# Kernel tuning notes

Hardware: AMD Instinct MI355X
Metric: run time of the kernel (lower is better)

Reference implementation:

```python
import jax, jax.numpy as jnp
import numpy as np

EPS = 1e-5

def ln(x, gamma, beta):
    m = jnp.mean(x, axis=-1, keepdims=True)
    std = jnp.sqrt(jnp.var(x, axis=-1, keepdims=True) + EPS)
    return gamma * ((x - m) / (std + EPS)) + beta

def hard_sigmoid(x):
    return jnp.clip(0.2 * x + 0.5, 0.0, 1.0)

def setup_inputs() -> dict:
    key = jax.random.key(0)
    B, T, D, U, UEP = 64, 2048, 256, 256, 64
    ks = jax.random.split(key, 16)
    def gn(k, shape, s=0.05):
        return (jax.random.normal(k, shape, dtype=jnp.float32) * s)
    inp = {}
    inp['x'] = jax.random.normal(ks[0], (B, T, D), dtype=jnp.float32)
    inp['mask'] = jax.random.randint(ks[1], (B, T), 0, 2, dtype=jnp.int32)
    inp['W'] = gn(ks[2], (D, 3 * U))
    inp['U'] = gn(ks[3], (U, 3 * U))
    inp['b'] = jnp.zeros((3 * U,), jnp.float32)
    inp['gammas'] = 1.0 + gn(ks[4], (2, 3 * U), 0.1)
    inp['betas'] = gn(ks[5], (2, 3 * U), 0.1)
    inp['W_EP'] = gn(ks[6], (D, 3 * UEP))
    inp['U_EP'] = gn(ks[7], (UEP, 3 * UEP))
    inp['b_EP'] = jnp.zeros((3 * UEP,), jnp.float32)
    inp['gammas_EP'] = 1.0 + gn(ks[8], (2, 3 * UEP), 0.1)
    inp['betas_EP'] = gn(ks[9], (2, 3 * UEP), 0.1)
    inp['W1_EP'] = gn(ks[10], (UEP, 1))
    inp['b1_EP'] = jnp.zeros((1,), jnp.float32)
    return inp

def _gru_step(s1, h_tm1, Umat, g1, bt1, dim):
    # s1: precomputed ln(x@W + b)  [B, 3*dim]
    s2 = ln(h_tm1 @ Umat[:, :2 * dim], g1[:2 * dim], bt1[:2 * dim])
    s = hard_sigmoid(s1[:, :2 * dim] + s2)
    z, r = s[:, :dim], s[:, dim:2 * dim]
    hh = ln((r * h_tm1) @ Umat[:, 2 * dim:], g1[2 * dim:], bt1[2 * dim:])
    return z * h_tm1 + (1.0 - z) * jnp.tanh(s1[:, 2 * dim:] + hh)

def _encoder(x, mask, W, U, b, gammas, betas, W_EP, U_EP, b_EP, gammas_EP, betas_EP, W1_EP, b1_EP):
    B, T, D = x.shape
    dim = U.shape[0]
    dim_ep = U_EP.shape[0]
    # input projections + their LayerNorms depend only on x -> precompute (same math)
    s1_all = ln(jnp.einsum('btd,dk->btk', x, W) + b, gammas[0], betas[0])          # [B,T,3U]
    s1_ep_all = ln(jnp.einsum('btd,dk->btk', x, W_EP) + b_EP, gammas_EP[0], betas_EP[0])  # [B,T,3Uep]
    s1_all = jnp.swapaxes(s1_all, 0, 1)        # [T,B,3U]
    s1_ep_all = jnp.swapaxes(s1_ep_all, 0, 1)  # [T,B,3Uep]
    xm_all = (mask > 0).T                      # [T,B] bool

    def step(carry, inp):
        h_tm1, hep_tm1, is_end_tm1 = carry
        s1, s1e, xm = inp
        h_tm1 = jnp.where(is_end_tm1[:, None] > 0.5, 0.0, h_tm1)
        h = _gru_step(s1, h_tm1, U, gammas[1], betas[1], dim)
        h = jnp.where(xm[:, None], h, h_tm1)
        hep = _gru_step(s1e, hep_tm1, U_EP, gammas_EP[1], betas_EP[1], dim_ep)
        hep = jnp.where(xm[:, None], hep, hep_tm1)
        is_end = jnp.round(jax.nn.sigmoid(hep_tm1 @ W1_EP + b1_EP))[:, 0]
        return (h, hep, is_end), (h, is_end)

    init = (jnp.zeros((B, dim), x.dtype), jnp.zeros((B, dim_ep), x.dtype), jnp.zeros((B,), x.dtype))
    _, (h_seq, end_seq) = jax.lax.scan(step, init, (s1_all, s1_ep_all, xm_all))
    return jnp.swapaxes(h_seq, 0, 1), jnp.swapaxes(end_seq, 0, 1)  # [B,T,U], [B,T]

def reference(x, mask, W, U, b, gammas, betas, W_EP, U_EP, b_EP, gammas_EP, betas_EP, W1_EP, b1_EP):
    return _encoder(x, mask, W, U, b, gammas, betas, W_EP, U_EP, b_EP, gammas_EP, betas_EP, W1_EP, b1_EP)
```

## Files before the change

### kernel.cpp

```cpp
#include <hip/hip_runtime.h>


typedef _Float16 h2  __attribute__((ext_vector_type(2)));
typedef _Float16 v8h __attribute__((ext_vector_type(8)));

__device__ __forceinline__ float fdot2_(h2 a, h2 b, float c) {
#if __has_builtin(__builtin_amdgcn_fdot2)
  return __builtin_amdgcn_fdot2(a, b, c, false);
#else
  return c + (float)a[0] * (float)b[0] + (float)a[1] * (float)b[1];
#endif
}

template <int I>
__device__ __forceinline__ h2 pr(v8h v) {
  h2 r; r[0] = v[2 * I]; r[1] = v[2 * I + 1]; return r;
}

__device__ __forceinline__ void wg_barrier() {
  __builtin_amdgcn_sched_barrier(0);
  asm volatile("s_waitcnt lgkmcnt(0)" ::: "memory");
  __builtin_amdgcn_sched_barrier(0);
  __builtin_amdgcn_s_barrier();
  __builtin_amdgcn_sched_barrier(0);
}

__global__ __launch_bounds__(256) void prep_kernel(
    const float* __restrict__ W, const float* __restrict__ U,
    const float* __restrict__ W_EP,
    _Float16* __restrict__ wt, _Float16* __restrict__ uzr,
    _Float16* __restrict__ uh, float* __restrict__ wept)
{
  const int blk = blockIdx.x;
  const int k = threadIdx.x;
  if (blk < 768) {
    const int j = blk;
    wt[(size_t)j * 256 + k] = (_Float16)W[(size_t)k * 768 + j];
  } else if (blk < 1280) {
    const int j = blk - 768;
    uzr[(size_t)j * 256 + k] = (_Float16)U[(size_t)k * 768 + j];
  } else if (blk < 1536) {
    const int j = blk - 1280;
    const int p = k >> 3, e = k & 7;
    uh[((size_t)p * 256 + j) * 8 + e] = (_Float16)U[(size_t)k * 768 + 512 + j];
  } else {
    const int j = blk - 1536;
    wept[(size_t)j * 256 + k] = W_EP[(size_t)k * 192 + j];
  }
}

__global__ __launch_bounds__(256) void ph1_main_kernel(
    const float* __restrict__ x, const _Float16* __restrict__ wt,
    const float* __restrict__ bvec, const float* __restrict__ gam,
    const float* __restrict__ bet, _Float16* __restrict__ s1out)
{
  __shared__ __align__(16) _Float16 xs[16][256];
  __shared__ float sp[16][768];
  const int tid = threadIdx.x;
  const size_t row0 = (size_t)blockIdx.x * 16;

  #pragma unroll
  for (int i = 0; i < 16; ++i)
    xs[i][tid] = (_Float16)x[(row0 + i) * 256 + tid];
  __syncthreads();

  #pragma unroll 1
  for (int cc = 0; cc < 3; ++cc) {
    const int col = cc * 256 + tid;
    const v8h* wp = (const v8h*)(wt + (size_t)col * 256);
    float acc[16];
    #pragma unroll
    for (int r = 0; r < 16; ++r) acc[r] = 0.f;
    #pragma unroll 4
    for (int c = 0; c < 32; ++c) {
      const v8h w8 = wp[c];
      #pragma unroll
      for (int r = 0; r < 16; ++r) {
        const v8h x8 = *(const v8h*)(&xs[r][c * 8]);
        acc[r] = fdot2_(pr<0>(x8), pr<0>(w8), acc[r]);
        acc[r] = fdot2_(pr<1>(x8), pr<1>(w8), acc[r]);
        acc[r] = fdot2_(pr<2>(x8), pr<2>(w8), acc[r]);
        acc[r] = fdot2_(pr<3>(x8), pr<3>(w8), acc[r]);
      }
    }
    const float bb = bvec[col];
    #pragma unroll
    for (int r = 0; r < 16; ++r) sp[r][col] = acc[r] + bb;
  }
  __syncthreads();

  const int w = tid >> 6, lane = tid & 63;
  for (int rr = 0; rr < 4; ++rr) {
    const int r = (w << 2) | rr;
    float vals[12], sum = 0.f, sq = 0.f;
    #pragma unroll
    for (int j = 0; j < 12; ++j) {
      const float v = sp[r][lane + (j << 6)];
      vals[j] = v; sum += v; sq += v * v;
    }
    #pragma unroll
    for (int m = 32; m >= 1; m >>= 1) {
      sum += __shfl_xor(sum, m); sq += __shfl_xor(sq, m);
    }
    const float mean = sum * (1.f / 768.f);
    const float var = sq * (1.f / 768.f) - mean * mean;
    const float inv = 1.f / (sqrtf(var + 1e-5f) + 1e-5f);
    #pragma unroll
    for (int j = 0; j < 12; ++j) {
      const int c = lane + (j << 6);
      s1out[(row0 + r) * 768 + c] =
          (_Float16)(gam[c] * ((vals[j] - mean) * inv) + bet[c]);
    }
  }
}

__global__ __launch_bounds__(192) void ph1_ep_kernel(
    const float* __restrict__ x, const float* __restrict__ wept,
    const float* __restrict__ bvec, const float* __restrict__ gam,
    const float* __restrict__ bet, void* __restrict__ s1e, const int store64)
{
  __shared__ __align__(16) float xs[16][256];
  __shared__ double sp[16][192];
  const int tid = threadIdx.x;
  const size_t row0 = (size_t)blockIdx.x * 16;

  for (int idx = tid; idx < 4096; idx += 192)
    xs[idx >> 8][idx & 255] = x[row0 * 256 + idx];
  __syncthreads();

  {
    const float4* wp = (const float4*)(wept + (size_t)tid * 256);
    double acc[16];
    #pragma unroll
    for (int r = 0; r < 16; ++r) acc[r] = 0.0;
    #pragma unroll 2
    for (int c = 0; c < 64; ++c) {
      const float4 w4 = wp[c];
      #pragma unroll
      for (int r = 0; r < 16; ++r) {
        const float4 x4 = *(const float4*)(&xs[r][c * 4]);
        acc[r] += (double)x4.x * (double)w4.x;
        acc[r] += (double)x4.y * (double)w4.y;
        acc[r] += (double)x4.z * (double)w4.z;
        acc[r] += (double)x4.w * (double)w4.w;
      }
    }
    const double bb = (double)bvec[tid];
    #pragma unroll
    for (int r = 0; r < 16; ++r) sp[r][tid] = acc[r] + bb;
  }
  __syncthreads();

  const int w = tid >> 6, lane = tid & 63;
  for (int r = w; r < 16; r += 3) {
    double vals[3], sum = 0.0, sq = 0.0;
    #pragma unroll
    for (int j = 0; j < 3; ++j) {
      const double v = sp[r][lane + (j << 6)];
      vals[j] = v; sum += v; sq += v * v;
    }
    #pragma unroll
    for (int m = 32; m >= 1; m >>= 1) {
      sum += __shfl_xor(sum, m); sq += __shfl_xor(sq, m);
    }
    const double mean = sum * (1.0 / 192.0);
    const double var = sq * (1.0 / 192.0) - mean * mean;
    const double den = sqrt(var + 1e-5) + 1e-5;
    #pragma unroll
    for (int j = 0; j < 3; ++j) {
      const int c = lane + (j << 6);
      const double vv = (double)gam[c] * ((vals[j] - mean) / den) + (double)bet[c];
      if (store64) ((double*)s1e)[(row0 + r) * 192 + c] = vv;
      else         ((float*)s1e)[(row0 + r) * 192 + c] = (float)vv;
    }
  }
}

#define OFF_UH     0
#define OFF_MASK   131072
#define OFF_HEP    139264
#define OFF_ZEE    139776
#define OFF_RHEP   140288
#define OFF_EPZRP  140800
#define OFF_EPHHP  140928
#define OFF_H2     140992
#define OFF_RH     141504
#define OFF_HF     142016
#define OFF_Z      143040
#define OFF_ZRP    144064
#define OFF_HHP    144128
#define OFF_FLAG   144160
#define SCAN_LDS_BYTES 144192

__global__ __launch_bounds__(512, 2) void scan_kernel(
    const _Float16* __restrict__ uzr_g, const _Float16* __restrict__ uh_g,
    const float* __restrict__ U_EP, const _Float16* __restrict__ s1,
    const void* __restrict__ s1e_v, const int s1e64,
    const int* __restrict__ mask,
    const float* __restrict__ gam1, const float* __restrict__ bet1,
    const float* __restrict__ gamep1, const float* __restrict__ betep1,
    const float* __restrict__ W1, const float* __restrict__ b1,
    float* __restrict__ out)
{
  extern __shared__ char sm[];
  const int t = threadIdx.x;
  const int b = blockIdx.x;
  const int w = t >> 6;
  const int je  = t >> 2;
  const int qe  = t & 3;
  const int jeh = (t & 255) >> 2;

  float*  hf    = (float*)(sm + OFF_HF);
  float*  flagp = (float*)(sm + OFF_FLAG);
  double* hepd  = (double*)(sm + OFF_HEP);
  int*    maskl = (int*)(sm + OFF_MASK);

  {
    const v8h* src = (const v8h*)uh_g;
    v8h* dst = (v8h*)(sm + OFF_UH);
    #pragma unroll
    for (int i = 0; i < 16; ++i) dst[i * 512 + t] = src[i * 512 + t];
  }
  #pragma unroll
  for (int i = 0; i < 4; ++i) maskl[i * 512 + t] = mask[((size_t)b << 11) + i * 512 + t];

  v8h uzrv[32];
  {
    const v8h* up = (const v8h*)uzr_g + (size_t)t * 32;
    #pragma unroll
    for (int c = 0; c < 32; ++c) uzrv[c] = up[c];
  }
  float uez[16], ueh[16];
  #pragma unroll
  for (int i = 0; i < 16; ++i) uez[i] = U_EP[(size_t)(16 * qe + i) * 192 + je];
  #pragma unroll
  for (int i = 0; i < 16; ++i) ueh[i] = U_EP[(size_t)(16 * qe + i) * 192 + 128 + jeh];

  const float gz = gam1[t],                bz = bet1[t];
  const float gh = gam1[512 + (t & 255)],  bh = bet1[512 + (t & 255)];
  const float gse = gamep1[je],            bse = betep1[je];
  const float ghe = gamep1[128 + jeh],     bhe = betep1[128 + jeh];
  const double w1d = (double)W1[t & 63];
  const double b1d = (double)b1[0];
  const double* dptr = (const double*)s1e_v;
  const float*  fptr = (const float*)s1e_v;

  if (t < 128) { h2 z2; z2[0] = (_Float16)0.f; z2[1] = (_Float16)0.f;
                 ((h2*)(sm + OFF_H2))[t] = z2; }
  if (t < 256) hf[t] = 0.f;
  if (t < 64)  hepd[t] = 0.0;
  if (t < 2)   flagp[t] = 0.f;

  const size_t n0 = (size_t)b << 11;
  float  s1zr_c = (float)s1[n0 * 768 + t];
  float  s1h_c  = (float)s1[n0 * 768 + 512 + (t & 255)];
  double s1ezr_c = s1e64 ? dptr[n0 * 192 + je]
                         : (double)fptr[n0 * 192 + je];
  double s1ehh_c = s1e64 ? dptr[n0 * 192 + 128 + jeh]
                         : (double)fptr[n0 * 192 + 128 + jeh];
  __syncthreads();

  for (int tt = 0; tt < 2048; ++tt) {
    const size_t n = ((size_t)b << 11) | (size_t)tt;
    const float fz = (flagp[tt & 1] > 0.5f) ? 0.f : 1.f;

    if (tt > 0 && t < 256) out[(n - 1) * 256 + t] = hf[t];

    const int ttn = (tt < 2047) ? tt + 1 : 2047;
    const size_t np1 = ((size_t)b << 11) | (size_t)ttn;
    const float  s1zr_n = (float)s1[np1 * 768 + t];
    const float  s1h_n  = (float)s1[np1 * 768 + 512 + (t & 255)];
    const double s1ezr_n = s1e64 ? dptr[np1 * 192 + je]
                                 : (double)fptr[np1 * 192 + je];
    const double s1ehh_n = s1e64 ? dptr[np1 * 192 + 128 + jeh]
                                 : (double)fptr[np1 * 192 + 128 + jeh];

    if (w == 7) {
      double p = hepd[t & 63] * w1d;
      #pragma unroll
      for (int m = 1; m <= 32; m <<= 1) p += __shfl_xor(p, m);
      if (t == 448) {
        const float e = ((p + b1d) > 0.0) ? 1.f : 0.f;
        flagp[(tt + 1) & 1] = e;
        out[(size_t)33554432 + n] = e;
      }
    }

    float d;
    {
      const v8h* hv = (const v8h*)(sm + OFF_H2);
      float a0 = 0.f, a1 = 0.f, a2 = 0.f, a3 = 0.f;
      #pragma unroll
      for (int c = 0; c < 32; ++c) {
        const v8h hc = hv[c];
        a0 = fdot2_(pr<0>(hc), pr<0>(uzrv[c]), a0);
        a1 = fdot2_(pr<1>(hc), pr<1>(uzrv[c]), a1);
        a2 = fdot2_(pr<2>(hc), pr<2>(uzrv[c]), a2);
        a3 = fdot2_(pr<3>(hc), pr<3>(uzrv[c]), a3);
      }
      d = ((a0 + a1) + (a2 + a3)) * fz;
      float s_ = d, q_ = d * d;
      #pragma unroll
      for (int m = 1; m <= 32; m <<= 1) { s_ += __shfl_xor(s_, m); q_ += __shfl_xor(q_, m); }
      if ((t & 63) == 0) ((float2*)(sm + OFF_ZRP))[w] = make_float2(s_, q_);
    }
    double de;
    {
      const double2* hp = (const double2*)(hepd + 16 * qe);
      double acc = 0.0;
      #pragma unroll
      for (int i = 0; i < 8; ++i) {
        const double2 hv2 = hp[i];
        acc += hv2.x * (double)uez[2 * i] + hv2.y * (double)uez[2 * i + 1];
      }
      acc += __shfl_xor(acc, 1); acc += __shfl_xor(acc, 2);
      de = acc;
      double es = de, eq = de * de;
      #pragma unroll
      for (int m = 4; m <= 32; m <<= 1) { es += __shfl_xor(es, m); eq += __shfl_xor(eq, m); }
      if ((t & 63) == 0) ((double2*)(sm + OFF_EPZRP))[w] = make_double2(es, eq);
    }
    wg_barrier();

    {
      float S = 0.f, Q = 0.f;
      const float4* zp = (const float4*)(sm + OFF_ZRP);
      #pragma unroll
      for (int i = 0; i < 4; ++i) { const float4 v = zp[i]; S += v.x + v.z; Q += v.y + v.w; }
      const float mean = S * (1.f / 512.f);
      const float var = Q * (1.f / 512.f) - mean * mean;
      const float inv = 1.f / (sqrtf(var + 1e-5f) + 1e-5f);
      const float s2v = gz * ((d - mean) * inv) + bz;
      float sv = 0.2f * (s1zr_c + s2v) + 0.5f;
      sv = fminf(fmaxf(sv, 0.f), 1.f);
      if (t < 256) ((float*)(sm + OFF_Z))[t] = sv;
      else {
        const float rhv = sv * (fz * hf[t - 256]);
        ((_Float16*)(sm + OFF_RH))[t - 256] = (_Float16)rhv;
      }
    }
    if ((t & 3) == 0) {
      double S = 0.0, Q = 0.0;
      const double2* ep = (const double2*)(sm + OFF_EPZRP);
      #pragma unroll
      for (int i = 0; i < 8; ++i) { S += ep[i].x; Q += ep[i].y; }
      const double mean = S * (1.0 / 128.0);
      const double var = Q * (1.0 / 128.0) - mean * mean;
      const double den = sqrt(var + 1e-5) + 1e-5;
      const double s2e = (double)gse * ((de - mean) / den) + (double)bse;
      double se = 0.2 * (s1ezr_c + s2e) + 0.5;
      se = fmin(fmax(se, 0.0), 1.0);
      if (je < 64) ((double*)(sm + OFF_ZEE))[je] = se;
      else         ((double*)(sm + OFF_RHEP))[je - 64] = se * hepd[je - 64];
    }
    wg_barrier();

    float dh = 0.f;
    double deh = 0.0;
    if (t < 256) {
      const v8h* rhv8 = (const v8h*)(sm + OFF_RH);
      const v8h* uhv  = (const v8h*)(sm + OFF_UH);
      float c0 = 0.f, c1 = 0.f, c2 = 0.f, c3 = 0.f;
      #pragma unroll
      for (int p = 0; p < 32; ++p) {
        const v8h rc = rhv8[p];
        const v8h uc = uhv[p * 256 + t];
        c0 = fdot2_(pr<0>(rc), pr<0>(uc), c0);
        c1 = fdot2_(pr<1>(rc), pr<1>(uc), c1);
        c2 = fdot2_(pr<2>(rc), pr<2>(uc), c2);
        c3 = fdot2_(pr<3>(rc), pr<3>(uc), c3);
      }
      dh = (c0 + c1) + (c2 + c3);
      float s_ = dh, q_ = dh * dh;
      #pragma unroll
      for (int m = 1; m <= 32; m <<= 1) { s_ += __shfl_xor(s_, m); q_ += __shfl_xor(q_, m); }
      if ((t & 63) == 0) ((float2*)(sm + OFF_HHP))[w] = make_float2(s_, q_);
    } else {
      const double2* rp = (const double2*)((double*)(sm + OFF_RHEP) + 16 * qe);
      double acc = 0.0;
      #pragma unroll
      for (int i = 0; i < 8; ++i) {
        const double2 rv = rp[i];
        acc += rv.x * (double)ueh[2 * i] + rv.y * (double)ueh[2 * i + 1];
      }
      acc += __shfl_xor(acc, 1); acc += __shfl_xor(acc, 2);
      deh = acc;
      double es = deh, eq = deh * deh;
      #pragma unroll
      for (int m = 4; m <= 32; m <<= 1) { es += __shfl_xor(es, m); eq += __shfl_xor(eq, m); }
      if ((t & 63) == 0) ((double2*)(sm + OFF_EPHHP))[w - 4] = make_double2(es, eq);
    }
    wg_barrier();

    const int xm = maskl[tt];
    if (t < 256) {
      float S = 0.f, Q = 0.f;
      const float4* hp4 = (const float4*)(sm + OFF_HHP);
      #pragma unroll
      for (int i = 0; i < 2; ++i) { const float4 v = hp4[i]; S += v.x + v.z; Q += v.y + v.w; }
      const float mean = S * (1.f / 256.f);
      const float var = Q * (1.f / 256.f) - mean * mean;
      const float inv = 1.f / (sqrtf(var + 1e-5f) + 1e-5f);
      const float hhv = gh * ((dh - mean) * inv) + bh;
      const float z = ((float*)(sm + OFF_Z))[t];
      const float hzf = fz * hf[t];
      const float hn = z * hzf + (1.f - z) * tanhf(s1h_c + hhv);
      const float hc_ = (xm > 0) ? hn : hzf;
      hf[t] = hc_;
      const float ho = __shfl_xor(hc_, 1);
      if (!(t & 1)) {
        h2 p2; p2[0] = (_Float16)hc_; p2[1] = (_Float16)ho;
        ((h2*)(sm + OFF_H2))[t >> 1] = p2;
      }
    } else if ((t & 3) == 0) {
      double S = 0.0, Q = 0.0;
      const double2* ep = (const double2*)(sm + OFF_EPHHP);
      #pragma unroll
      for (int i = 0; i < 4; ++i) { S += ep[i].x; Q += ep[i].y; }
      const double mean = S * (1.0 / 64.0);
      const double var = Q * (1.0 / 64.0) - mean * mean;
      const double den = sqrt(var + 1e-5) + 1e-5;
      const double hhe = (double)ghe * ((deh - mean) / den) + (double)bhe;
      const double ze = ((double*)(sm + OFF_ZEE))[jeh];
      const double hold = hepd[jeh];
      const double hepn = ze * hold + (1.0 - ze) * tanh(s1ehh_c + hhe);
      hepd[jeh] = (xm > 0) ? hepn : hold;
    }
    wg_barrier();

    s1zr_c = s1zr_n; s1h_c = s1h_n; s1ezr_c = s1ezr_n; s1ehh_c = s1ehh_n;
  }
  if (t < 256) out[((((size_t)b << 11) | 2047)) * 256 + t] = hf[t];
}

extern "C" void kernel_launch(void* const* d_in, const int* in_sizes, int n_in,
                              void* d_out, int out_size, void* d_ws, size_t ws_size,
                              hipStream_t stream)
{
  (void)in_sizes; (void)n_in; (void)out_size;
  const float* x       = (const float*)d_in[0];
  const int*   mask    = (const int*)d_in[1];
  const float* W       = (const float*)d_in[2];
  const float* U       = (const float*)d_in[3];
  const float* bvec    = (const float*)d_in[4];
  const float* gammas  = (const float*)d_in[5];
  const float* betas   = (const float*)d_in[6];
  const float* W_EP    = (const float*)d_in[7];
  const float* U_EP    = (const float*)d_in[8];
  const float* b_EP    = (const float*)d_in[9];
  const float* gammasE = (const float*)d_in[10];
  const float* betasE  = (const float*)d_in[11];
  const float* W1_EP   = (const float*)d_in[12];
  const float* b1_EP   = (const float*)d_in[13];
  float* out = (float*)d_out;

  const size_t NR = 131072;
  const size_t S1_SZ    = NR * 768 * 2;
  const size_t S1E64_SZ = NR * 192 * 8;
  const size_t S1E32_SZ = NR * 192 * 4;
  const size_t WSMALL = 262144 + 131072 + 393216 + 196608;
  const int s1e64 = (ws_size >= S1_SZ + S1E64_SZ + WSMALL) ? 1 : 0;
  const size_t S1E_SZ = s1e64 ? S1E64_SZ : S1E32_SZ;
  if (ws_size < S1_SZ + S1E32_SZ + WSMALL) return;

  char* ws = (char*)d_ws;
  size_t off = 0;
  void* s1e      = (void*)(ws + off);      off += S1E_SZ;
  _Float16* s1   = (_Float16*)(ws + off);  off += S1_SZ;
  _Float16* uzr  = (_Float16*)(ws + off);  off += 262144;
  _Float16* uh   = (_Float16*)(ws + off);  off += 131072;
  _Float16* wt   = (_Float16*)(ws + off);  off += 393216;
  float* wept    = (float*)(ws + off);     off += 196608;

  prep_kernel<<<dim3(1728), dim3(256), 0, stream>>>(
      W, U, W_EP, wt, uzr, uh, wept);
  ph1_main_kernel<<<dim3(8192), dim3(256), 0, stream>>>(
      x, wt, bvec, gammas, betas, s1);
  ph1_ep_kernel<<<dim3(8192), dim3(192), 0, stream>>>(
      x, wept, b_EP, gammasE, betasE, s1e, s1e64);

  hipFuncSetAttribute(reinterpret_cast<const void*>(scan_kernel),
                      hipFuncAttributeMaxDynamicSharedMemorySize, SCAN_LDS_BYTES);
  scan_kernel<<<dim3(64), dim3(512), SCAN_LDS_BYTES, stream>>>(
      uzr, uh, U_EP, s1, (const void*)s1e, s1e64, mask,
      gammas + 768, betas + 768, gammasE + 192, betasE + 192,
      W1_EP, b1_EP, out);
}
```

Before: 20.75 ms.

## Stream recurrent weights from global each step and broadcast hidden state via readlane

The 512-lane register cache of the z/r recurrent weights (32 v8h per thread) is dropped. Each step now reloads those weights from global/L2 in two halves of 16 vectors, interleaved with the EP dot product and the end-flag computation. The hidden state and r*h vectors are read once per lane from LDS and broadcast with readlane, replacing repeated LDS vector loads. This frees a large block of VGPRs, but it adds per-step global traffic on the serial critical path and many scalar readlane operations.

```diff
diff --git a/kernel.cpp b/kernel.cpp
--- a/kernel.cpp
+++ b/kernel.cpp
@@ -15,6 +15,10 @@
 template <int I>
 __device__ __forceinline__ h2 pr(v8h v) {
   h2 r; r[0] = v[2 * I]; r[1] = v[2 * I + 1]; return r;
+}
+
+__device__ __forceinline__ h2 rl2(int wreg, int k) {
+  return __builtin_bit_cast(h2, __builtin_amdgcn_readlane(wreg, k));
 }
 
 __device__ __forceinline__ void wg_barrier() {
@@ -206,6 +210,7 @@
   const int t = threadIdx.x;
   const int b = blockIdx.x;
   const int w = t >> 6;
+  const int lane = t & 63;
   const int je  = t >> 2;
   const int qe  = t & 3;
   const int jeh = (t & 255) >> 2;
@@ -224,12 +229,6 @@
   #pragma unroll
   for (int i = 0; i < 4; ++i) maskl[i * 512 + t] = mask[((size_t)b << 11) + i * 512 + t];
 
-  v8h uzrv[32];
-  {
-    const v8h* up = (const v8h*)uzr_g + (size_t)t * 32;
-    #pragma unroll
-    for (int c = 0; c < 32; ++c) uzrv[c] = up[c];
-  }
   float uez[16], ueh[16];
   #pragma unroll
   for (int i = 0; i < 16; ++i) uez[i] = U_EP[(size_t)(16 * qe + i) * 192 + je];
@@ -240,10 +239,11 @@
   const float gh = gam1[512 + (t & 255)],  bh = bet1[512 + (t & 255)];
   const float gse = gamep1[je],            bse = betep1[je];
   const float ghe = gamep1[128 + jeh],     bhe = betep1[128 + jeh];
-  const double w1d = (double)W1[t & 63];
+  const double w1d = (double)W1[lane];
   const double b1d = (double)b1[0];
   const double* dptr = (const double*)s1e_v;
   const float*  fptr = (const float*)s1e_v;
+  const v8h* up = (const v8h*)uzr_g + (size_t)t * 32;
 
   if (t < 128) { h2 z2; z2[0] = (_Float16)0.f; z2[1] = (_Float16)0.f;
                  ((h2*)(sm + OFF_H2))[t] = z2; }
@@ -266,6 +266,10 @@
 
     if (tt > 0 && t < 256) out[(n - 1) * 256 + t] = hf[t];
 
+    v8h wz[16];
+    #pragma unroll
+    for (int c = 0; c < 16; ++c) wz[c] = up[c];
+
     const int ttn = (tt < 2047) ? tt + 1 : 2047;
     const size_t np1 = ((size_t)b << 11) | (size_t)ttn;
     const float  s1zr_n = (float)s1[np1 * 768 + t];
@@ -275,41 +279,35 @@
     const double s1ehh_n = s1e64 ? dptr[np1 * 192 + 128 + jeh]
                                  : (double)fptr[np1 * 192 + 128 + jeh];
 
-    if (w == 7) {
-      double p = hepd[t & 63] * w1d;
-      #pragma unroll
-      for (int m = 1; m <= 32; m <<= 1) p += __shfl_xor(p, m);
-      if (t == 448) {
-        const float e = ((p + b1d) > 0.0) ? 1.f : 0.f;
-        flagp[(tt + 1) & 1] = e;
-        out[(size_t)33554432 + n] = e;
-      }
-    }
-
-    float d;
-    {
-      const v8h* hv = (const v8h*)(sm + OFF_H2);
-      float a0 = 0.f, a1 = 0.f, a2 = 0.f, a3 = 0.f;
-      #pragma unroll
-      for (int c = 0; c < 32; ++c) {
-        const v8h hc = hv[c];
-        a0 = fdot2_(pr<0>(hc), pr<0>(uzrv[c]), a0);
-        a1 = fdot2_(pr<1>(hc), pr<1>(uzrv[c]), a1);
-        a2 = fdot2_(pr<2>(hc), pr<2>(uzrv[c]), a2);
-        a3 = fdot2_(pr<3>(hc), pr<3>(uzrv[c]), a3);
-      }
-      d = ((a0 + a1) + (a2 + a3)) * fz;
-      float s_ = d, q_ = d * d;
-      #pragma unroll
-      for (int m = 1; m <= 32; m <<= 1) { s_ += __shfl_xor(s_, m); q_ += __shfl_xor(q_, m); }
-      if ((t & 63) == 0) ((float2*)(sm + OFF_ZRP))[w] = make_float2(s_, q_);
-    }
+    const int* h2i = (const int*)(sm + OFF_H2);
+    const int hw0 = h2i[lane];
+    const int hw1 = h2i[64 + lane];
+
     double de;
     {
       const double2* hp = (const double2*)(hepd + 16 * qe);
       double acc = 0.0;
       #pragma unroll
-      for (int i = 0; i < 8; ++i) {
+      for (int i = 0; i < 4; ++i) {
+        const double2 hv2 = hp[i];
+        acc += hv2.x * (double)uez[2 * i] + hv2.y * (double)uez[2 * i + 1];
+      }
+
+      float a0 = 0.f, a1 = 0.f, a2 = 0.f, a3 = 0.f;
+      #pragma unroll
+      for (int c = 0; c < 16; ++c) {
+        const v8h wv = wz[c];
+        a0 = fdot2_(rl2(hw0, 4 * c + 0), pr<0>(wv), a0);
+        a1 = fdot2_(rl2(hw0, 4 * c + 1), pr<1>(wv), a1);
+        a2 = fdot2_(rl2(hw0, 4 * c + 2), pr<2>(wv), a2);
+        a3 = fdot2_(rl2(hw0, 4 * c + 3), pr<3>(wv), a3);
+      }
+
+      #pragma unroll
+      for (int c = 0; c < 16; ++c) wz[c] = up[16 + c];
+
+      #pragma unroll
+      for (int i = 4; i < 8; ++i) {
         const double2 hv2 = hp[i];
         acc += hv2.x * (double)uez[2 * i] + hv2.y * (double)uez[2 * i + 1];
       }
@@ -318,63 +316,99 @@
       double es = de, eq = de * de;
       #pragma unroll
       for (int m = 4; m <= 32; m <<= 1) { es += __shfl_xor(es, m); eq += __shfl_xor(eq, m); }
-      if ((t & 63) == 0) ((double2*)(sm + OFF_EPZRP))[w] = make_double2(es, eq);
-    }
-    wg_barrier();
-
-    {
-      float S = 0.f, Q = 0.f;
-      const float4* zp = (const float4*)(sm + OFF_ZRP);
-      #pragma unroll
-      for (int i = 0; i < 4; ++i) { const float4 v = zp[i]; S += v.x + v.z; Q += v.y + v.w; }
-      const float mean = S * (1.f / 512.f);
-      const float var = Q * (1.f / 512.f) - mean * mean;
-      const float inv = 1.f / (sqrtf(var + 1e-5f) + 1e-5f);
-      const float s2v = gz * ((d - mean) * inv) + bz;
-      float sv = 0.2f * (s1zr_c + s2v) + 0.5f;
-      sv = fminf(fmaxf(sv, 0.f), 1.f);
-      if (t < 256) ((float*)(sm + OFF_Z))[t] = sv;
-      else {
-        const float rhv = sv * (fz * hf[t - 256]);
-        ((_Float16*)(sm + OFF_RH))[t - 256] = (_Float16)rhv;
-      }
-    }
-    if ((t & 3) == 0) {
-      double S = 0.0, Q = 0.0;
-      const double2* ep = (const double2*)(sm + OFF_EPZRP);
-      #pragma unroll
-      for (int i = 0; i < 8; ++i) { S += ep[i].x; Q += ep[i].y; }
-      const double mean = S * (1.0 / 128.0);
-      const double var = Q * (1.0 / 128.0) - mean * mean;
-      const double den = sqrt(var + 1e-5) + 1e-5;
-      const double s2e = (double)gse * ((de - mean) / den) + (double)bse;
-      double se = 0.2 * (s1ezr_c + s2e) + 0.5;
-      se = fmin(fmax(se, 0.0), 1.0);
-      if (je < 64) ((double*)(sm + OFF_ZEE))[je] = se;
-      else         ((double*)(sm + OFF_RHEP))[je - 64] = se * hepd[je - 64];
+      if (lane == 0) ((double2*)(sm + OFF_EPZRP))[w] = make_double2(es, eq);
+
+      if (w == 7) {
+        double p = hepd[lane] * w1d;
+        #pragma unroll
+        for (int m = 1; m <= 32; m <<= 1) p += __shfl_xor(p, m);
+        if (t == 448) {
+          const float e = ((p + b1d) > 0.0) ? 1.f : 0.f;
+          flagp[(tt + 1) & 1] = e;
+          out[(size_t)33554432 + n] = e;
+        }
+      }
+
+      #pragma unroll
+      for (int c = 0; c < 16; ++c) {
+        const v8h wv = wz[c];
+        a0 = fdot2_(rl2(hw1, 4 * c + 0), pr<0>(wv), a0);
+        a1 = fdot2_(rl2(hw1, 4 * c + 1), pr<1>(wv), a1);
+        a2 = fdot2_(rl2(hw1, 4 * c + 2), pr<2>(wv), a2);
+        a3 = fdot2_(rl2(hw1, 4 * c + 3), pr<3>(wv), a3);
+      }
+      const float d_ = ((a0 + a1) + (a2 + a3)) * fz;
+      float s_ = d_, q_ = d_ * d_;
+      #pragma unroll
+      for (int m = 1; m <= 32; m <<= 1) { s_ += __shfl_xor(s_, m); q_ += __shfl_xor(q_, m); }
+      if (lane == 0) ((float2*)(sm + OFF_ZRP))[w] = make_float2(s_, q_);
+
+      s_ = d_;
+      wg_barrier();
+
+      {
+        float S = 0.f, Q = 0.f;
+        const float4* zp = (const float4*)(sm + OFF_ZRP);
+        #pragma unroll
+        for (int i = 0; i < 4; ++i) { const float4 v = zp[i]; S += v.x + v.z; Q += v.y + v.w; }
+        const float mean = S * (1.f / 512.f);
+        const float var = Q * (1.f / 512.f) - mean * mean;
+        const float inv = 1.f / (sqrtf(var + 1e-5f) + 1e-5f);
+        const float s2v = gz * ((d_ - mean) * inv) + bz;
+        float sv = 0.2f * (s1zr_c + s2v) + 0.5f;
+        sv = fminf(fmaxf(sv, 0.f), 1.f);
+        if (t < 256) ((float*)(sm + OFF_Z))[t] = sv;
+        else {
+          const float rhv = sv * (fz * hf[t - 256]);
+          ((_Float16*)(sm + OFF_RH))[t - 256] = (_Float16)rhv;
+        }
+      }
+      if ((t & 3) == 0) {
+        double S = 0.0, Q = 0.0;
+        const double2* ep = (const double2*)(sm + OFF_EPZRP);
+        #pragma unroll
+        for (int i = 0; i < 8; ++i) { S += ep[i].x; Q += ep[i].y; }
+        const double mean = S * (1.0 / 128.0);
+        const double var = Q * (1.0 / 128.0) - mean * mean;
+        const double den = sqrt(var + 1e-5) + 1e-5;
+        const double s2e = (double)gse * ((de - mean) / den) + (double)bse;
+        double se = 0.2 * (s1ezr_c + s2e) + 0.5;
+        se = fmin(fmax(se, 0.0), 1.0);
+        if (je < 64) ((double*)(sm + OFF_ZEE))[je] = se;
+        else         ((double*)(sm + OFF_RHEP))[je - 64] = se * hepd[je - 64];
+      }
     }
     wg_barrier();
 
     float dh = 0.f;
     double deh = 0.0;
     if (t < 256) {
-      const v8h* rhv8 = (const v8h*)(sm + OFF_RH);
-      const v8h* uhv  = (const v8h*)(sm + OFF_UH);
+      const int* rhi = (const int*)(sm + OFF_RH);
+      const int rr0 = rhi[lane];
+      const int rr1 = rhi[64 + lane];
+      const v8h* uhv = (const v8h*)(sm + OFF_UH);
       float c0 = 0.f, c1 = 0.f, c2 = 0.f, c3 = 0.f;
       #pragma unroll
-      for (int p = 0; p < 32; ++p) {
-        const v8h rc = rhv8[p];
+      for (int p = 0; p < 16; ++p) {
         const v8h uc = uhv[p * 256 + t];
-        c0 = fdot2_(pr<0>(rc), pr<0>(uc), c0);
-        c1 = fdot2_(pr<1>(rc), pr<1>(uc), c1);
-        c2 = fdot2_(pr<2>(rc), pr<2>(uc), c2);
-        c3 = fdot2_(pr<3>(rc), pr<3>(uc), c3);
+        c0 = fdot2_(rl2(rr0, 4 * p + 0), pr<0>(uc), c0);
+        c1 = fdot2_(rl2(rr0, 4 * p + 1), pr<1>(uc), c1);
+        c2 = fdot2_(rl2(rr0, 4 * p + 2), pr<2>(uc), c2);
+        c3 = fdot2_(rl2(rr0, 4 * p + 3), pr<3>(uc), c3);
+      }
+      #pragma unroll
+      for (int p = 16; p < 32; ++p) {
+        const v8h uc = uhv[p * 256 + t];
+        c0 = fdot2_(rl2(rr1, 4 * (p - 16) + 0), pr<0>(uc), c0);
+        c1 = fdot2_(rl2(rr1, 4 * (p - 16) + 1), pr<1>(uc), c1);
+        c2 = fdot2_(rl2(rr1, 4 * (p - 16) + 2), pr<2>(uc), c2);
+        c3 = fdot2_(rl2(rr1, 4 * (p - 16) + 3), pr<3>(uc), c3);
       }
       dh = (c0 + c1) + (c2 + c3);
       float s_ = dh, q_ = dh * dh;
       #pragma unroll
       for (int m = 1; m <= 32; m <<= 1) { s_ += __shfl_xor(s_, m); q_ += __shfl_xor(q_, m); }
-      if ((t & 63) == 0) ((float2*)(sm + OFF_HHP))[w] = make_float2(s_, q_);
+      if (lane == 0) ((float2*)(sm + OFF_HHP))[w] = make_float2(s_, q_);
     } else {
       const double2* rp = (const double2*)((double*)(sm + OFF_RHEP) + 16 * qe);
       double acc = 0.0;
@@ -388,7 +422,7 @@
       double es = deh, eq = deh * deh;
       #pragma unroll
       for (int m = 4; m <= 32; m <<= 1) { es += __shfl_xor(es, m); eq += __shfl_xor(eq, m); }
-      if ((t & 63) == 0) ((double2*)(sm + OFF_EPHHP))[w - 4] = make_double2(es, eq);
+      if (lane == 0) ((double2*)(sm + OFF_EPHHP))[w - 4] = make_double2(es, eq);
     }
     wg_barrier();
 
```

New measurement: 16.76 ms. 19.2% less time.

## Halve scan workgroup to 256 threads, stream U_zr weights from global each step

Applied to the files above, without the earlier changes.

The recurrent scan kernel now runs with 256 threads instead of 512. Each thread computes both the z and r gate columns, and the EP path handles two gate columns per thread. The U_zr weights are no longer held in registers. They are re-read from global memory (L2) every timestep through a software-pipelined triple-buffered load/dot sequence, using a new interleaved layout. The aim is to cut barrier and cross-wave reduction cost per step with fewer waves. The tradeoff is double the per-thread dot-product work and weight bandwidth on the serial critical path.

```diff
diff --git a/kernel.cpp b/kernel.cpp
--- a/kernel.cpp
+++ b/kernel.cpp
@@ -23,6 +23,32 @@
   __builtin_amdgcn_sched_barrier(0);
   __builtin_amdgcn_s_barrier();
   __builtin_amdgcn_sched_barrier(0);
+}
+
+template <int K>
+__device__ __forceinline__ void ldblk(v8h* d, const v8h* base, int tz, int tr) {
+  #pragma unroll
+  for (int i = 0; i < 4; ++i) {
+    d[i]     = base[(size_t)(4 * K + i) * 512 + tz];
+    d[4 + i] = base[(size_t)(4 * K + i) * 512 + tr];
+  }
+}
+template <int K>
+__device__ __forceinline__ void dotblk(const v8h* hv, const v8h* d,
+    float& za0, float& za1, float& za2, float& za3,
+    float& ra0, float& ra1, float& ra2, float& ra3) {
+  #pragma unroll
+  for (int i = 0; i < 4; ++i) {
+    const v8h hc = hv[4 * K + i];
+    za0 = fdot2_(pr<0>(hc), pr<0>(d[i]), za0);
+    za1 = fdot2_(pr<1>(hc), pr<1>(d[i]), za1);
+    za2 = fdot2_(pr<2>(hc), pr<2>(d[i]), za2);
+    za3 = fdot2_(pr<3>(hc), pr<3>(d[i]), za3);
+    ra0 = fdot2_(pr<0>(hc), pr<0>(d[4 + i]), ra0);
+    ra1 = fdot2_(pr<1>(hc), pr<1>(d[4 + i]), ra1);
+    ra2 = fdot2_(pr<2>(hc), pr<2>(d[4 + i]), ra2);
+    ra3 = fdot2_(pr<3>(hc), pr<3>(d[4 + i]), ra3);
+  }
 }
 
 __global__ __launch_bounds__(256) void prep_kernel(
@@ -38,7 +64,8 @@
     wt[(size_t)j * 256 + k] = (_Float16)W[(size_t)k * 768 + j];
   } else if (blk < 1280) {
     const int j = blk - 768;
-    uzr[(size_t)j * 256 + k] = (_Float16)U[(size_t)k * 768 + j];
+    const int c = k >> 3, e = k & 7;
+    uzr[((size_t)c * 512 + j) * 8 + e] = (_Float16)U[(size_t)k * 768 + j];
   } else if (blk < 1536) {
     const int j = blk - 1280;
     const int p = k >> 3, e = k & 7;
@@ -186,13 +213,12 @@
 #define OFF_H2     140992
 #define OFF_RH     141504
 #define OFF_HF     142016
-#define OFF_Z      143040
 #define OFF_ZRP    144064
 #define OFF_HHP    144128
 #define OFF_FLAG   144160
 #define SCAN_LDS_BYTES 144192
 
-__global__ __launch_bounds__(512, 2) void scan_kernel(
+__global__ __launch_bounds__(256, 1) void scan_kernel(
     const _Float16* __restrict__ uzr_g, const _Float16* __restrict__ uh_g,
     const float* __restrict__ U_EP, const _Float16* __restrict__ s1,
     const void* __restrict__ s1e_v, const int s1e64,
@@ -206,9 +232,9 @@
   const int t = threadIdx.x;
   const int b = blockIdx.x;
   const int w = t >> 6;
+  const int lane = t & 63;
+  const int qe  = t & 3;
   const int je  = t >> 2;
-  const int qe  = t & 3;
-  const int jeh = (t & 255) >> 2;
 
   float*  hf    = (float*)(sm + OFF_HF);
   float*  flagp = (float*)(sm + OFF_FLAG);
@@ -219,145 +245,157 @@
     const v8h* src = (const v8h*)uh_g;
     v8h* dst = (v8h*)(sm + OFF_UH);
     #pragma unroll
-    for (int i = 0; i < 16; ++i) dst[i * 512 + t] = src[i * 512 + t];
-  }
-  #pragma unroll
-  for (int i = 0; i < 4; ++i) maskl[i * 512 + t] = mask[((size_t)b << 11) + i * 512 + t];
-
-  v8h uzrv[32];
-  {
-    const v8h* up = (const v8h*)uzr_g + (size_t)t * 32;
-    #pragma unroll
-    for (int c = 0; c < 32; ++c) uzrv[c] = up[c];
-  }
-  float uez[16], ueh[16];
-  #pragma unroll
-  for (int i = 0; i < 16; ++i) uez[i] = U_EP[(size_t)(16 * qe + i) * 192 + je];
-  #pragma unroll
-  for (int i = 0; i < 16; ++i) ueh[i] = U_EP[(size_t)(16 * qe + i) * 192 + 128 + jeh];
-
-  const float gz = gam1[t],                bz = bet1[t];
-  const float gh = gam1[512 + (t & 255)],  bh = bet1[512 + (t & 255)];
-  const float gse = gamep1[je],            bse = betep1[je];
-  const float ghe = gamep1[128 + jeh],     bhe = betep1[128 + jeh];
-  const double w1d = (double)W1[t & 63];
+    for (int i = 0; i < 32; ++i) dst[i * 256 + t] = src[i * 256 + t];
+  }
+  #pragma unroll
+  for (int i = 0; i < 8; ++i) maskl[i * 256 + t] = mask[((size_t)b << 11) + i * 256 + t];
+
+  float uezA[16], uezB[16], ueh[16];
+  #pragma unroll
+  for (int i = 0; i < 16; ++i) uezA[i] = U_EP[(size_t)(16 * qe + i) * 192 + je];
+  #pragma unroll
+  for (int i = 0; i < 16; ++i) uezB[i] = U_EP[(size_t)(16 * qe + i) * 192 + 64 + je];
+  #pragma unroll
+  for (int i = 0; i < 16; ++i) ueh[i] = U_EP[(size_t)(16 * qe + i) * 192 + 128 + je];
+
+  const float gz  = gam1[t],        bz  = bet1[t];
+  const float gzr = gam1[256 + t],  bzr = bet1[256 + t];
+  const float gh  = gam1[512 + t],  bh  = bet1[512 + t];
+  const float gseA = gamep1[je],       bseA = betep1[je];
+  const float gseB = gamep1[64 + je],  bseB = betep1[64 + je];
+  const float ghe  = gamep1[128 + je], bhe  = betep1[128 + je];
+  const double w1d = (double)W1[lane];
   const double b1d = (double)b1[0];
   const double* dptr = (const double*)s1e_v;
   const float*  fptr = (const float*)s1e_v;
 
   if (t < 128) { h2 z2; z2[0] = (_Float16)0.f; z2[1] = (_Float16)0.f;
                  ((h2*)(sm + OFF_H2))[t] = z2; }
-  if (t < 256) hf[t] = 0.f;
+  hf[t] = 0.f;
   if (t < 64)  hepd[t] = 0.0;
   if (t < 2)   flagp[t] = 0.f;
 
   const size_t n0 = (size_t)b << 11;
-  float  s1zr_c = (float)s1[n0 * 768 + t];
-  float  s1h_c  = (float)s1[n0 * 768 + 512 + (t & 255)];
-  double s1ezr_c = s1e64 ? dptr[n0 * 192 + je]
-                         : (double)fptr[n0 * 192 + je];
-  double s1ehh_c = s1e64 ? dptr[n0 * 192 + 128 + jeh]
-                         : (double)fptr[n0 * 192 + 128 + jeh];
+  float  s1zA_c = (float)s1[n0 * 768 + t];
+  float  s1zB_c = (float)s1[n0 * 768 + 256 + t];
+  float  s1h_c  = (float)s1[n0 * 768 + 512 + t];
+  double s1eA_c = s1e64 ? dptr[n0 * 192 + je]      : (double)fptr[n0 * 192 + je];
+  double s1eB_c = s1e64 ? dptr[n0 * 192 + 64 + je] : (double)fptr[n0 * 192 + 64 + je];
+  double s1eh_c = s1e64 ? dptr[n0 * 192 + 128 + je]: (double)fptr[n0 * 192 + 128 + je];
   __syncthreads();
 
   for (int tt = 0; tt < 2048; ++tt) {
     const size_t n = ((size_t)b << 11) | (size_t)tt;
     const float fz = (flagp[tt & 1] > 0.5f) ? 0.f : 1.f;
 
-    if (tt > 0 && t < 256) out[(n - 1) * 256 + t] = hf[t];
+    if (tt > 0) out[(n - 1) * 256 + t] = hf[t];
 
     const int ttn = (tt < 2047) ? tt + 1 : 2047;
     const size_t np1 = ((size_t)b << 11) | (size_t)ttn;
-    const float  s1zr_n = (float)s1[np1 * 768 + t];
-    const float  s1h_n  = (float)s1[np1 * 768 + 512 + (t & 255)];
-    const double s1ezr_n = s1e64 ? dptr[np1 * 192 + je]
-                                 : (double)fptr[np1 * 192 + je];
-    const double s1ehh_n = s1e64 ? dptr[np1 * 192 + 128 + jeh]
-                                 : (double)fptr[np1 * 192 + 128 + jeh];
-
-    if (w == 7) {
-      double p = hepd[t & 63] * w1d;
+    const float  s1zA_n = (float)s1[np1 * 768 + t];
+    const float  s1zB_n = (float)s1[np1 * 768 + 256 + t];
+    const float  s1h_n  = (float)s1[np1 * 768 + 512 + t];
+    const double s1eA_n = s1e64 ? dptr[np1 * 192 + je]       : (double)fptr[np1 * 192 + je];
+    const double s1eB_n = s1e64 ? dptr[np1 * 192 + 64 + je]  : (double)fptr[np1 * 192 + 64 + je];
+    const double s1eh_n = s1e64 ? dptr[np1 * 192 + 128 + je] : (double)fptr[np1 * 192 + 128 + je];
+
+    const v8h* uzb = (const v8h*)uzr_g;
+    asm volatile("" : "+v"(uzb));
+    v8h A[8], Bv[8], Cv[8];
+    ldblk<0>(A, uzb, t, 256 + t);
+    ldblk<1>(Bv, uzb, t, 256 + t);
+    ldblk<2>(Cv, uzb, t, 256 + t);
+
+    const v8h* hv = (const v8h*)(sm + OFF_H2);
+    float za0 = 0.f, za1 = 0.f, za2 = 0.f, za3 = 0.f;
+    float ra0 = 0.f, ra1 = 0.f, ra2 = 0.f, ra3 = 0.f;
+    dotblk<0>(hv, A,  za0, za1, za2, za3, ra0, ra1, ra2, ra3);
+    ldblk<3>(A, uzb, t, 256 + t);
+    dotblk<1>(hv, Bv, za0, za1, za2, za3, ra0, ra1, ra2, ra3);
+    ldblk<4>(Bv, uzb, t, 256 + t);
+    dotblk<2>(hv, Cv, za0, za1, za2, za3, ra0, ra1, ra2, ra3);
+    ldblk<5>(Cv, uzb, t, 256 + t);
+    dotblk<3>(hv, A,  za0, za1, za2, za3, ra0, ra1, ra2, ra3);
+    ldblk<6>(A, uzb, t, 256 + t);
+    dotblk<4>(hv, Bv, za0, za1, za2, za3, ra0, ra1, ra2, ra3);
+    ldblk<7>(Bv, uzb, t, 256 + t);
+
+    double deA, deB;
+    {
+      const double2* hp = (const double2*)(hepd + 16 * qe);
+      double accA = 0.0, accB = 0.0;
+      #pragma unroll
+      for (int i = 0; i < 8; ++i) {
+        const double2 hv2 = hp[i];
+        accA += hv2.x * (double)uezA[2 * i] + hv2.y * (double)uezA[2 * i + 1];
+        accB += hv2.x * (double)uezB[2 * i] + hv2.y * (double)uezB[2 * i + 1];
+      }
+      accA += __shfl_xor(accA, 1); accA += __shfl_xor(accA, 2);
+      accB += __shfl_xor(accB, 1); accB += __shfl_xor(accB, 2);
+      deA = accA; deB = accB;
+      double es = deA + deB, eq = deA * deA + deB * deB;
+      #pragma unroll
+      for (int m = 4; m <= 32; m <<= 1) { es += __shfl_xor(es, m); eq += __shfl_xor(eq, m); }
+      if (lane == 0) ((double2*)(sm + OFF_EPZRP))[w] = make_double2(es, eq);
+    }
+    if (w == 3) {
+      double p = hepd[lane] * w1d;
       #pragma unroll
       for (int m = 1; m <= 32; m <<= 1) p += __shfl_xor(p, m);
-      if (t == 448) {
+      if (t == 192) {
         const float e = ((p + b1d) > 0.0) ? 1.f : 0.f;
         flagp[(tt + 1) & 1] = e;
         out[(size_t)33554432 + n] = e;
       }
     }
 
-    float d;
+    dotblk<5>(hv, Cv, za0, za1, za2, za3, ra0, ra1, ra2, ra3);
+    dotblk<6>(hv, A,  za0, za1, za2, za3, ra0, ra1, ra2, ra3);
+    dotblk<7>(hv, Bv, za0, za1, za2, za3, ra0, ra1, ra2, ra3);
+    const float dz = ((za0 + za1) + (za2 + za3)) * fz;
+    const float dr = ((ra0 + ra1) + (ra2 + ra3)) * fz;
     {
-      const v8h* hv = (const v8h*)(sm + OFF_H2);
-      float a0 = 0.f, a1 = 0.f, a2 = 0.f, a3 = 0.f;
-      #pragma unroll
-      for (int c = 0; c < 32; ++c) {
-        const v8h hc = hv[c];
-        a0 = fdot2_(pr<0>(hc), pr<0>(uzrv[c]), a0);
-        a1 = fdot2_(pr<1>(hc), pr<1>(uzrv[c]), a1);
-        a2 = fdot2_(pr<2>(hc), pr<2>(uzrv[c]), a2);
-        a3 = fdot2_(pr<3>(hc), pr<3>(uzrv[c]), a3);
-      }
-      d = ((a0 + a1) + (a2 + a3)) * fz;
-      float s_ = d, q_ = d * d;
+      float s_ = dz + dr, q_ = dz * dz + dr * dr;
       #pragma unroll
       for (int m = 1; m <= 32; m <<= 1) { s_ += __shfl_xor(s_, m); q_ += __shfl_xor(q_, m); }
-      if ((t & 63) == 0) ((float2*)(sm + OFF_ZRP))[w] = make_float2(s_, q_);
-    }
-    double de;
-    {
-      const double2* hp = (const double2*)(hepd + 16 * qe);
-      double acc = 0.0;
-      #pragma unroll
-      for (int i = 0; i < 8; ++i) {
-        const double2 hv2 = hp[i];
-        acc += hv2.x * (double)uez[2 * i] + hv2.y * (double)uez[2 * i + 1];
-      }
-      acc += __shfl_xor(acc, 1); acc += __shfl_xor(acc, 2);
-      de = acc;
-      double es = de, eq = de * de;
-      #pragma unroll
-      for (int m = 4; m <= 32; m <<= 1) { es += __shfl_xor(es, m); eq += __shfl_xor(eq, m); }
-      if ((t & 63) == 0) ((double2*)(sm + OFF_EPZRP))[w] = make_double2(es, eq);
+      if (lane == 0) ((float2*)(sm + OFF_ZRP))[w] = make_float2(s_, q_);
     }
     wg_barrier();
 
+    float zreg;
     {
       float S = 0.f, Q = 0.f;
       const float4* zp = (const float4*)(sm + OFF_ZRP);
       #pragma unroll
-      for (int i = 0; i < 4; ++i) { const float4 v = zp[i]; S += v.x + v.z; Q += v.y + v.w; }
+      for (int i = 0; i < 2; ++i) { const float4 v = zp[i]; S += v.x + v.z; Q += v.y + v.w; }
       const float mean = S * (1.f / 512.f);
       const float var = Q * (1.f / 512.f) - mean * mean;
       const float inv = 1.f / (sqrtf(var + 1e-5f) + 1e-5f);
-      const float s2v = gz * ((d - mean) * inv) + bz;
-      float sv = 0.2f * (s1zr_c + s2v) + 0.5f;
-      sv = fminf(fmaxf(sv, 0.f), 1.f);
-      if (t < 256) ((float*)(sm + OFF_Z))[t] = sv;
-      else {
-        const float rhv = sv * (fz * hf[t - 256]);
-        ((_Float16*)(sm + OFF_RH))[t - 256] = (_Float16)rhv;
-      }
-    }
-    if ((t & 3) == 0) {
+      float sz = 0.2f * (s1zA_c + (gz * ((dz - mean) * inv) + bz)) + 0.5f;
+      zreg = fminf(fmaxf(sz, 0.f), 1.f);
+      float sr = 0.2f * (s1zB_c + (gzr * ((dr - mean) * inv) + bzr)) + 0.5f;
+      sr = fminf(fmaxf(sr, 0.f), 1.f);
+      ((_Float16*)(sm + OFF_RH))[t] = (_Float16)(sr * (fz * hf[t]));
+    }
+    if (qe == 0) {
       double S = 0.0, Q = 0.0;
       const double2* ep = (const double2*)(sm + OFF_EPZRP);
       #pragma unroll
-      for (int i = 0; i < 8; ++i) { S += ep[i].x; Q += ep[i].y; }
+      for (int i = 0; i < 4; ++i) { S += ep[i].x; Q += ep[i].y; }
       const double mean = S * (1.0 / 128.0);
       const double var = Q * (1.0 / 128.0) - mean * mean;
       const double den = sqrt(var + 1e-5) + 1e-5;
-      const double s2e = (double)gse * ((de - mean) / den) + (double)bse;
-      double se = 0.2 * (s1ezr_c + s2e) + 0.5;
-      se = fmin(fmax(se, 0.0), 1.0);
-      if (je < 64) ((double*)(sm + OFF_ZEE))[je] = se;
-      else         ((double*)(sm + OFF_RHEP))[je - 64] = se * hepd[je - 64];
+      double seA = 0.2 * (s1eA_c + ((double)gseA * ((deA - mean) / den) + (double)bseA)) + 0.5;
+      seA = fmin(fmax(seA, 0.0), 1.0);
+      ((double*)(sm + OFF_ZEE))[je] = seA;
+      double seB = 0.2 * (s1eB_c + ((double)gseB * ((deB - mean) / den) + (double)bseB)) + 0.5;
+      seB = fmin(fmax(seB, 0.0), 1.0);
+      ((double*)(sm + OFF_RHEP))[je] = seB * hepd[je];
     }
     wg_barrier();
 
-    float dh = 0.f;
-    double deh = 0.0;
-    if (t < 256) {
+    float dh;
+    {
       const v8h* rhv8 = (const v8h*)(sm + OFF_RH);
       const v8h* uhv  = (const v8h*)(sm + OFF_UH);
       float c0 = 0.f, c1 = 0.f, c2 = 0.f, c3 = 0.f;
@@ -374,8 +412,10 @@
       float s_ = dh, q_ = dh * dh;
       #pragma unroll
       for (int m = 1; m <= 32; m <<= 1) { s_ += __shfl_xor(s_, m); q_ += __shfl_xor(q_, m); }
-      if ((t & 63) == 0) ((float2*)(sm + OFF_HHP))[w] = make_float2(s_, q_);
-    } else {
+      if (lane == 0) ((float2*)(sm + OFF_HHP))[w] = make_float2(s_, q_);
+    }
+    double deh;
+    {
       const double2* rp = (const double2*)((double*)(sm + OFF_RHEP) + 16 * qe);
       double acc = 0.0;
       #pragma unroll
@@ -388,12 +428,12 @@
       double es = deh, eq = deh * deh;
       #pragma unroll
       for (int m = 4; m <= 32; m <<= 1) { es += __shfl_xor(es, m); eq += __shfl_xor(eq, m); }
-      if ((t & 63) == 0) ((double2*)(sm + OFF_EPHHP))[w - 4] = make_double2(es, eq);
+      if (lane == 0) ((double2*)(sm + OFF_EPHHP))[w] = make_double2(es, eq);
     }
     wg_barrier();
 
     const int xm = maskl[tt];
-    if (t < 256) {
+    {
       float S = 0.f, Q = 0.f;
       const float4* hp4 = (const float4*)(sm + OFF_HHP);
       #pragma unroll
@@ -402,9 +442,8 @@
       const float var = Q * (1.f / 256.f) - mean * mean;
       const float inv = 1.f / (sqrtf(var + 1e-5f) + 1e-5f);
       const float hhv = gh * ((dh - mean) * inv) + bh;
-      const float z = ((float*)(sm + OFF_Z))[t];
       const float hzf = fz * hf[t];
-      const float hn = z * hzf + (1.f - z) * tanhf(s1h_c + hhv);
+      const float hn = zreg * hzf + (1.f - zreg) * tanhf(s1h_c + hhv);
       const float hc_ = (xm > 0) ? hn : hzf;
       hf[t] = hc_;
       const float ho = __shfl_xor(hc_, 1);
@@ -412,7 +451,8 @@
         h2 p2; p2[0] = (_Float16)hc_; p2[1] = (_Float16)ho;
         ((h2*)(sm + OFF_H2))[t >> 1] = p2;
       }
-    } else if ((t & 3) == 0) {
+    }
+    if (qe == 0) {
       double S = 0.0, Q = 0.0;
       const double2* ep = (const double2*)(sm + OFF_EPHHP);
       #pragma unroll
@@ -421,16 +461,17 @@
       const double var = Q * (1.0 / 64.0) - mean * mean;
       const double den = sqrt(var + 1e-5) + 1e-5;
       const double hhe = (double)ghe * ((deh - mean) / den) + (double)bhe;
-      const double ze = ((double*)(sm + OFF_ZEE))[jeh];
-      const double hold = hepd[jeh];
-      const double hepn = ze * hold + (1.0 - ze) * tanh(s1ehh_c + hhe);
-      hepd[jeh] = (xm > 0) ? hepn : hold;
+      const double ze = ((double*)(sm + OFF_ZEE))[je];
+      const double hold = hepd[je];
+      const double hepn = ze * hold + (1.0 - ze) * tanh(s1eh_c + hhe);
+      hepd[je] = (xm > 0) ? hepn : hold;
     }
     wg_barrier();
 
-    s1zr_c = s1zr_n; s1h_c = s1h_n; s1ezr_c = s1ezr_n; s1ehh_c = s1ehh_n;
-  }
-  if (t < 256) out[((((size_t)b << 11) | 2047)) * 256 + t] = hf[t];
+    s1zA_c = s1zA_n; s1zB_c = s1zB_n; s1h_c = s1h_n;
+    s1eA_c = s1eA_n; s1eB_c = s1eB_n; s1eh_c = s1eh_n;
+  }
+  out[((((size_t)b << 11) | 2047)) * 256 + t] = hf[t];
 }
 
 extern "C" void kernel_launch(void* const* d_in, const int* in_sizes, int n_in,
@@ -481,7 +522,7 @@
 
   hipFuncSetAttribute(reinterpret_cast<const void*>(scan_kernel),
                       hipFuncAttributeMaxDynamicSharedMemorySize, SCAN_LDS_BYTES);
-  scan_kernel<<<dim3(64), dim3(512), SCAN_LDS_BYTES, stream>>>(
+  scan_kernel<<<dim3(64), dim3(256), SCAN_LDS_BYTES, stream>>>(
       uzr, uh, U_EP, s1, (const void*)s1e, s1e64, mask,
       gammas + 768, betas + 768, gammasE + 192, betasE + 192,
       W1_EP, b1_EP, out);
```

Result: slower. 23.48 ms (+13.2%).

## Stream recurrent U_zr weights from global each step instead of holding in registers

Applied to the files above, without the earlier changes.

The 32 v8h recurrent z/r weight registers per thread are no longer kept resident. Each timestep instead streams them from global/L2 memory through an 8-entry double buffer, and the prep kernel reorders uzr into a coalesced chunk-major layout to suit this. The EP dot product is split and interleaved with the streamed loads to hide their latency. The aim is to cut register pressure, which may raise occupancy or avoid spills. The cost is reading about 256KB of weights per step per block, which adds L2 bandwidth demand and latency on the serial recurrence.

```diff
diff --git a/kernel.cpp b/kernel.cpp
--- a/kernel.cpp
+++ b/kernel.cpp
@@ -38,7 +38,8 @@
     wt[(size_t)j * 256 + k] = (_Float16)W[(size_t)k * 768 + j];
   } else if (blk < 1280) {
     const int j = blk - 768;
-    uzr[(size_t)j * 256 + k] = (_Float16)U[(size_t)k * 768 + j];
+    const int c = k >> 3, e = k & 7;
+    uzr[((size_t)c * 512 + j) * 8 + e] = (_Float16)U[(size_t)k * 768 + j];
   } else if (blk < 1536) {
     const int j = blk - 1280;
     const int p = k >> 3, e = k & 7;
@@ -224,12 +225,6 @@
   #pragma unroll
   for (int i = 0; i < 4; ++i) maskl[i * 512 + t] = mask[((size_t)b << 11) + i * 512 + t];
 
-  v8h uzrv[32];
-  {
-    const v8h* up = (const v8h*)uzr_g + (size_t)t * 32;
-    #pragma unroll
-    for (int c = 0; c < 32; ++c) uzrv[c] = up[c];
-  }
   float uez[16], ueh[16];
   #pragma unroll
   for (int i = 0; i < 16; ++i) uez[i] = U_EP[(size_t)(16 * qe + i) * 192 + je];
@@ -266,6 +261,15 @@
 
     if (tt > 0 && t < 256) out[(n - 1) * 256 + t] = hf[t];
 
+    const v8h* uzb = (const v8h*)uzr_g;
+    asm volatile("" : "+v"(uzb));
+
+    v8h wbuf[8];
+    #pragma unroll
+    for (int q = 0; q < 4; ++q) wbuf[q]     = uzb[(size_t)q * 512 + t];
+    #pragma unroll
+    for (int q = 0; q < 4; ++q) wbuf[4 + q] = uzb[(size_t)(4 + q) * 512 + t];
+
     const int ttn = (tt < 2047) ? tt + 1 : 2047;
     const size_t np1 = ((size_t)b << 11) | (size_t)ttn;
     const float  s1zr_n = (float)s1[np1 * 768 + t];
@@ -286,39 +290,57 @@
       }
     }
 
-    float d;
+    double de;
+    const double2* hp = (const double2*)(hepd + 16 * qe);
     {
-      const v8h* hv = (const v8h*)(sm + OFF_H2);
-      float a0 = 0.f, a1 = 0.f, a2 = 0.f, a3 = 0.f;
-      #pragma unroll
-      for (int c = 0; c < 32; ++c) {
-        const v8h hc = hv[c];
-        a0 = fdot2_(pr<0>(hc), pr<0>(uzrv[c]), a0);
-        a1 = fdot2_(pr<1>(hc), pr<1>(uzrv[c]), a1);
-        a2 = fdot2_(pr<2>(hc), pr<2>(uzrv[c]), a2);
-        a3 = fdot2_(pr<3>(hc), pr<3>(uzrv[c]), a3);
-      }
-      d = ((a0 + a1) + (a2 + a3)) * fz;
+      double acc = 0.0;
+      #pragma unroll
+      for (int i = 0; i < 4; ++i) {
+        const double2 hv2 = hp[i];
+        acc += hv2.x * (double)uez[2 * i] + hv2.y * (double)uez[2 * i + 1];
+      }
+      de = acc;
+    }
+
+    const v8h* hv = (const v8h*)(sm + OFF_H2);
+    float a0 = 0.f, a1 = 0.f, a2 = 0.f, a3 = 0.f;
+    #pragma unroll
+    for (int k = 0; k < 8; ++k) {
+      #pragma unroll
+      for (int i = 0; i < 4; ++i) {
+        const v8h hc = hv[4 * k + i];
+        const v8h wz = wbuf[(k & 1) * 4 + i];
+        a0 = fdot2_(pr<0>(hc), pr<0>(wz), a0);
+        a1 = fdot2_(pr<1>(hc), pr<1>(wz), a1);
+        a2 = fdot2_(pr<2>(hc), pr<2>(wz), a2);
+        a3 = fdot2_(pr<3>(hc), pr<3>(wz), a3);
+      }
+      if (k < 6) {
+        #pragma unroll
+        for (int q = 0; q < 4; ++q)
+          wbuf[(k & 1) * 4 + q] = uzb[(size_t)(4 * (k + 2) + q) * 512 + t];
+      }
+      if (k == 3) {
+        double acc = de;
+        #pragma unroll
+        for (int i = 4; i < 8; ++i) {
+          const double2 hv2 = hp[i];
+          acc += hv2.x * (double)uez[2 * i] + hv2.y * (double)uez[2 * i + 1];
+        }
+        acc += __shfl_xor(acc, 1); acc += __shfl_xor(acc, 2);
+        de = acc;
+        double es = de, eq = de * de;
+        #pragma unroll
+        for (int m = 4; m <= 32; m <<= 1) { es += __shfl_xor(es, m); eq += __shfl_xor(eq, m); }
+        if ((t & 63) == 0) ((double2*)(sm + OFF_EPZRP))[w] = make_double2(es, eq);
+      }
+    }
+    const float d = ((a0 + a1) + (a2 + a3)) * fz;
+    {
       float s_ = d, q_ = d * d;
       #pragma unroll
       for (int m = 1; m <= 32; m <<= 1) { s_ += __shfl_xor(s_, m); q_ += __shfl_xor(q_, m); }
       if ((t & 63) == 0) ((float2*)(sm + OFF_ZRP))[w] = make_float2(s_, q_);
-    }
-    double de;
-    {
-      const double2* hp = (const double2*)(hepd + 16 * qe);
-      double acc = 0.0;
-      #pragma unroll
-      for (int i = 0; i < 8; ++i) {
-        const double2 hv2 = hp[i];
-        acc += hv2.x * (double)uez[2 * i] + hv2.y * (double)uez[2 * i + 1];
-      }
-      acc += __shfl_xor(acc, 1); acc += __shfl_xor(acc, 2);
-      de = acc;
-      double es = de, eq = de * de;
-      #pragma unroll
-      for (int m = 4; m <= 32; m <<= 1) { es += __shfl_xor(es, m); eq += __shfl_xor(eq, m); }
-      if ((t & 63) == 0) ((double2*)(sm + OFF_EPZRP))[w] = make_double2(es, eq);
     }
     wg_barrier();
 
```

Result: faster. 18.94 ms (-8.7%).
